# Optimization experiments

Hardware: AMD Instinct MI355X
Metric: run time of the kernel (lower is better)

## Reference

```python
import jax, jax.numpy as jnp
import numpy as np

N, E, T, R, L = 100000, 800000, 2, 4, 2
DIN, H, C, DOUT = 16, 256, 128, 4
EPS = 1e-5


def hetero_linear(x, node_type, W, b):
    # y[i] = x[i] @ W[node_type[i]] + b[node_type[i]]; small fixed T loop
    out = jnp.zeros((x.shape[0], W.shape[-1]), x.dtype)
    for t in range(W.shape[0]):
        out = out + jnp.where((node_type == t)[:, None], x @ W[t] + b[t], jnp.zeros((), x.dtype))
    return out


def hetero_bn(x, node_type, gamma, beta):
    # per-node-type batch norm (training-mode statistics, biased variance)
    T_ = gamma.shape[0]
    cnt = jax.ops.segment_sum(jnp.ones((x.shape[0],), x.dtype), node_type, num_segments=T_)
    cnt = jnp.maximum(cnt, 1.0)[:, None]
    mean = jax.ops.segment_sum(x, node_type, num_segments=T_) / cnt
    var = jax.ops.segment_sum(x * x, node_type, num_segments=T_) / cnt - mean * mean
    inv = jax.lax.rsqrt(var + EPS)
    return (x - mean[node_type]) * inv[node_type] * gamma[node_type] + beta[node_type]


def rgcn_conv(x, edge_index, edge_type, W, root, bias):
    # RGCNConv with sum aggregation: out_i = x_i @ root + b + sum_{(j->i), r} x_j @ W_r
    src, dst = edge_index[0], edge_index[1]
    hs = jnp.einsum('nd,rdf->rnf', x, W)          # [R, N, C]
    msg = hs[edge_type, src]                       # [E, C] per-edge relation-transformed source feats
    agg = jax.ops.segment_sum(msg, dst, num_segments=x.shape[0])
    return agg + x @ root + bias


def setup_inputs() -> dict:
    key = jax.random.key(0)
    ks = iter(jax.random.split(key, 40))

    def w(shape, fan_in):
        return jax.random.normal(next(ks), shape, jnp.float32) / np.float32(np.sqrt(fan_in))

    inp = {}
    inp['x'] = jax.random.normal(next(ks), (N, DIN), jnp.float32)
    inp['edge_index'] = jax.random.randint(next(ks), (2, E), 0, N)
    inp['node_type'] = jax.random.randint(next(ks), (N,), 0, T)
    inp['edge_type'] = jax.random.randint(next(ks), (E,), 0, R)
    inp['ri_w0'] = w((T, DIN, H), DIN); inp['ri_b0'] = jnp.zeros((T, H))
    inp['ri_g0'] = jnp.ones((T, H)); inp['ri_be0'] = jnp.zeros((T, H))
    inp['ri_w1'] = w((T, H, C), H); inp['ri_b1'] = jnp.zeros((T, C))
    inp['cn_g'] = jnp.ones((L, T, C)); inp['cn_b'] = jnp.zeros((L, T, C))
    inp['rg_w'] = w((L, R, C, C), C); inp['rg_root'] = w((L, C, C), C); inp['rg_bias'] = jnp.zeros((L, C))
    inp['mn_g'] = jnp.ones((L, T, C)); inp['mn_b'] = jnp.zeros((L, T, C))
    inp['mw0'] = w((L, T, C, H), C); inp['mb0'] = jnp.zeros((L, T, H))
    inp['mg0'] = jnp.ones((L, T, H)); inp['mbe0'] = jnp.zeros((L, T, H))
    inp['mw1'] = w((L, T, H, C), H); inp['mb1'] = jnp.zeros((L, T, C))
    inp['ro_w0'] = w((T, C, H), C); inp['ro_b0'] = jnp.zeros((T, H))
    inp['ro_g0'] = jnp.ones((T, H)); inp['ro_be0'] = jnp.zeros((T, H))
    inp['ro_w1'] = w((T, H, DOUT), H); inp['ro_b1'] = jnp.zeros((T, DOUT))
    return inp


def reference(x, edge_index, node_type, edge_type,
              ri_w0, ri_b0, ri_g0, ri_be0, ri_w1, ri_b1,
              cn_g, cn_b, rg_w, rg_root, rg_bias,
              mn_g, mn_b, mw0, mb0, mg0, mbe0, mw1, mb1,
              ro_w0, ro_b0, ro_g0, ro_be0, ro_w1, ro_b1):
    act = jax.nn.leaky_relu  # negative_slope 0.01, as nn.LeakyReLU default
    # readin MLP (plain_last)
    h = hetero_linear(x, node_type, ri_w0, ri_b0)
    h = act(hetero_bn(h, node_type, ri_g0, ri_be0))
    h = hetero_linear(h, node_type, ri_w1, ri_b1)
    # RES+ blocks: Norm -> Act -> Conv -> +res, Norm -> Act -> MLP -> +res (dropout=0)
    for l in range(rg_w.shape[0]):
        y = act(hetero_bn(h, node_type, cn_g[l], cn_b[l]))
        h = h + rgcn_conv(y, edge_index, edge_type, rg_w[l], rg_root[l], rg_bias[l])
        y = act(hetero_bn(h, node_type, mn_g[l], mn_b[l]))
        y = hetero_linear(y, node_type, mw0[l], mb0[l])
        y = act(hetero_bn(y, node_type, mg0[l], mbe0[l]))
        y = hetero_linear(y, node_type, mw1[l], mb1[l])
        h = h + y
    # readout MLP (plain_last)
    h = hetero_linear(h, node_type, ro_w0, ro_b0)
    h = act(hetero_bn(h, node_type, ro_g0, ro_be0))
    return hetero_linear(h, node_type, ro_w1, ro_b1)
```

## Files before the change

### kernel.cpp

```cpp
#include <hip/hip_runtime.h>

#define TT 2
#define RR 4
#define LL 2
#define DIN 16
#define HH 256
#define CC 128
#define DOUT 4
#define EPS 1e-5f
#define NB 32
#define NBG 16

typedef float v4f __attribute__((ext_vector_type(4)));
typedef short bf16x8 __attribute__((ext_vector_type(8)));

__device__ __forceinline__ ushort f2bf(float x) {
    uint u = __float_as_uint(x);
    return (ushort)((u + 0x7fffu + ((u >> 16) & 1u)) >> 16);
}
__device__ __forceinline__ float bf2f(ushort h) { return __uint_as_float(((uint)h) << 16); }
__device__ __forceinline__ int swc(int c) { return c ^ ((c >> 3) & 7); }
__device__ __forceinline__ uint pack2(float x, float y) {
    return (uint)f2bf(x) | ((uint)f2bf(y) << 16);
}

__global__ __launch_bounds__(1024) void k_scan1(const int* __restrict__ in, int* __restrict__ out,
                                                int* __restrict__ part, int n) {
    __shared__ int sm[1024];
    const int tid = threadIdx.x;
    const int i = blockIdx.x * 1024 + tid;
    const int v = (i < n) ? in[i] : 0;
    sm[tid] = v;
    __syncthreads();
    for (int off = 1; off < 1024; off <<= 1) {
        const int u = (tid >= off) ? sm[tid - off] : 0;
        __syncthreads();
        sm[tid] += u;
        __syncthreads();
    }
    if (i < n) out[i] = sm[tid] - v;
    if (tid == 1023) part[blockIdx.x] = sm[1023];
}

__global__ __launch_bounds__(1024) void k_scan2(int* __restrict__ part, int nb) {
    __shared__ int sm[1024];
    const int tid = threadIdx.x;
    const int v = (tid < nb) ? part[tid] : 0;
    sm[tid] = v;
    __syncthreads();
    for (int off = 1; off < 1024; off <<= 1) {
        const int u = (tid >= off) ? sm[tid - off] : 0;
        __syncthreads();
        sm[tid] += u;
        __syncthreads();
    }
    if (tid < nb) part[tid] = sm[tid] - v;
    if (tid == nb - 1) part[nb] = sm[tid];
}

__global__ __launch_bounds__(1024) void k_scan3(int* __restrict__ arr, const int* __restrict__ part,
                                                int n, int nb, int* __restrict__ typeStart,
                                                int* __restrict__ out2) {
    const int i = blockIdx.x * 1024 + threadIdx.x;
    if (i < n) {
        const int v = arr[i] + part[i >> 10];
        arr[i] = v;
        if (out2) out2[i] = v;
    } else if (i == n) {
        const int total = part[nb];
        arr[n] = total;
        if (typeStart) { typeStart[0] = 0; typeStart[1] = n - total; typeStart[2] = n; }
    }
}

__global__ __launch_bounds__(256) void k_build_perm(const int* __restrict__ nt, const int* __restrict__ pscan,
                                                    const int* __restrict__ typeStart, int* __restrict__ perm,
                                                    int* __restrict__ inv, int n) {
    const int i = blockIdx.x * 256 + threadIdx.x;
    if (i >= n) return;
    const int s1 = pscan[i];
    const int pos = nt[i] ? (typeStart[1] + s1) : (i - s1);
    perm[pos] = i;
    inv[i] = pos;
}

__global__ __launch_bounds__(256) void k_deg2(const int* __restrict__ dstv, const int* __restrict__ et,
                                              const int* __restrict__ inv, int* __restrict__ rowp2, int nE) {
    const int e = blockIdx.x * 256 + threadIdx.x;
    if (e < nE) atomicAdd(&rowp2[inv[dstv[e]] * 4 + et[e]], 1);
}

__global__ __launch_bounds__(256) void k_fill2(const int* __restrict__ srcv, const int* __restrict__ dstv,
                                               const int* __restrict__ et, const int* __restrict__ inv,
                                               int* __restrict__ cur, int* __restrict__ csr, int nE) {
    const int e = blockIdx.x * 256 + threadIdx.x;
    if (e < nE) {
        const int pos = atomicAdd(&cur[inv[dstv[e]] * 4 + et[e]], 1);
        csr[pos] = inv[srcv[e]];
    }
}

__global__ __launch_bounds__(256) void k_packall(const float* __restrict__ ri_w1, const float* __restrict__ mw0,
                                                 const float* __restrict__ mw1, const float* __restrict__ ro_w0,
                                                 ushort* __restrict__ p_ri1, ushort* __restrict__ p_mw0,
                                                 ushort* __restrict__ p_mw1, ushort* __restrict__ p_ro0) {
    for (long long idx = (long long)blockIdx.x * 256 + threadIdx.x; idx < 393216;
         idx += (long long)gridDim.x * 256) {
        const float* src; ushort* dst; int K, N; long long lo;
        if (idx < 65536)       { src = ri_w1; dst = p_ri1; K = 256; N = 128; lo = idx; }
        else if (idx < 196608) { src = mw0;   dst = p_mw0; K = 128; N = 256; lo = idx - 65536; }
        else if (idx < 327680) { src = mw1;   dst = p_mw1; K = 256; N = 128; lo = idx - 196608; }
        else                   { src = ro_w0; dst = p_ro0; K = 128; N = 256; lo = idx - 327680; }
        const int kn = K * N;
        const int mat = (int)(lo / kn);
        const int rem = (int)(lo - (long long)mat * kn);
        const int k = rem / N, col = rem % N;
        dst[((size_t)mat * (K / 8) + (k >> 3)) * N * 8 + (size_t)col * 8 + (k & 7)] = f2bf(src[lo]);
    }
}

__global__ __launch_bounds__(256) void k_pack_conv(const float* __restrict__ rgw_all,
                                                   const float* __restrict__ root_all,
                                                   ushort* __restrict__ dst_all) {
    const int idx = blockIdx.x * 256 + threadIdx.x;
    if (idx >= 640 * 128) return;
    const int l = blockIdx.y;
    const float* rgw = rgw_all + (size_t)l * RR * CC * CC;
    const float* root = root_all + (size_t)l * CC * CC;
    ushort* dst = dst_all + (size_t)l * 640 * 128;
    const int k = idx >> 7, col = idx & 127;
    const float v = (k < 512) ? rgw[(((k >> 7) * CC) + (k & 127)) * CC + col]
                              : root[(size_t)(k - 512) * CC + col];
    dst[((size_t)(k >> 3) * CC + col) * 8 + (k & 7)] = f2bf(v);
}

__global__ __launch_bounds__(512) void k_coef(const float* __restrict__ stat, const int* __restrict__ typeStart,
                                              const float* __restrict__ g, const float* __restrict__ be,
                                              float* __restrict__ scale, float* __restrict__ shift, int F) {
    const int tid = threadIdx.x;
    if (tid >= TT * F) return;
    const int t = tid / F;
    float s = 0.f, q = 0.f;
    for (int b = 0; b < NB; ++b) {
        s += stat[(size_t)b * 1024 + tid];
        q += stat[(size_t)b * 1024 + 512 + tid];
    }
    const float cnt = fmaxf((float)(typeStart[t + 1] - typeStart[t]), 1.f);
    const float mean = s / cnt;
    const float var = q / cnt - mean * mean;
    const float sc = g[tid] * rsqrtf(var + EPS);
    scale[tid] = sc;
    shift[tid] = be[tid] - mean * sc;
}

__global__ __launch_bounds__(256) void k_bnact(const float* __restrict__ h, const float* __restrict__ stat_in,
                                               const float* __restrict__ gg, const float* __restrict__ bb,
                                               const int* __restrict__ typeStart,
                                               ushort* __restrict__ y16, int n) {
    __shared__ float scs[2 * CC];
    __shared__ float sfs[2 * CC];
    const int tid = threadIdx.x;
    for (int idx = tid; idx < 2 * CC; idx += 256) {
        const int t = idx >> 7;
        float s = 0.f, q = 0.f;
        for (int b = 0; b < NB; ++b) {
            s += stat_in[(size_t)b * 1024 + idx];
            q += stat_in[(size_t)b * 1024 + 512 + idx];
        }
        const float cnt = fmaxf((float)(typeStart[t + 1] - typeStart[t]), 1.f);
        const float mean = s / cnt;
        const float var = q / cnt - mean * mean;
        const float sc = gg[idx] * rsqrtf(var + EPS);
        scs[idx] = sc;
        sfs[idx] = bb[idx] - mean * sc;
    }
    __syncthreads();
    const int c0 = typeStart[1];
    const long long total = (long long)n * 32;
    for (long long idx = (long long)blockIdx.x * 256 + threadIdx.x; idx < total;
         idx += (long long)gridDim.x * 256) {
        const int i = (int)(idx >> 5), cq = (int)(idx & 31);
        const int tb = (i >= c0) ? CC : 0;
        const v4f v = *(const v4f*)(h + (size_t)i * CC + cq * 4);
        float o[4];
#pragma unroll
        for (int j = 0; j < 4; ++j) {
            const float vv = fmaf(v[j], scs[tb + cq * 4 + j], sfs[tb + cq * 4 + j]);
            o[j] = fmaxf(vv, 0.01f * vv);
        }
        uint2 p = make_uint2(pack2(o[0], o[1]), pack2(o[2], o[3]));
        *(uint2*)((uint*)y16 + (size_t)i * 64 + cq * 2) = p;
    }
}

__global__ __launch_bounds__(256) void k_agg4(const ushort* __restrict__ y16, const int* __restrict__ rowp2,
                                              const int* __restrict__ csr, ushort* __restrict__ buf,
                                              int q0, int q1) {
    const int wid = threadIdx.x >> 6, lane = threadIdx.x & 63;
    const int i = q0 + blockIdx.x * 4 + wid;
    if (i >= q1) return;
    const uint* y32 = (const uint*)y16;
    float2 a0 = {0.f, 0.f}, a1 = {0.f, 0.f}, a2 = {0.f, 0.f}, a3 = {0.f, 0.f};
    const int e0 = rowp2[4 * i], b1 = rowp2[4 * i + 1], b2 = rowp2[4 * i + 2],
              b3 = rowp2[4 * i + 3], e1 = rowp2[4 * i + 4];
    for (int base = e0; base < e1; base += 64) {
        const int cnt = min(64, e1 - base);
        int pk = (lane < cnt) ? csr[base + lane] : 0;
        for (int j = 0; j < cnt; j += 8) {
            const int m = min(8, cnt - j);
            uint u[8];
#pragma unroll
            for (int k = 0; k < 8; ++k) {
                if (k < m) {
                    const int s = __shfl(pk, j + k);
                    u[k] = y32[(size_t)s * 64 + lane];
                }
            }
#pragma unroll
            for (int k = 0; k < 8; ++k) {
                if (k < m) {
                    const int idx = base + j + k;
                    const float vx = bf2f((ushort)(u[k] & 0xffff));
                    const float vy = bf2f((ushort)(u[k] >> 16));
                    if (idx < b1)      { a0.x += vx; a0.y += vy; }
                    else if (idx < b2) { a1.x += vx; a1.y += vy; }
                    else if (idx < b3) { a2.x += vx; a2.y += vy; }
                    else               { a3.x += vx; a3.y += vy; }
                }
            }
        }
    }
    uint* brow = (uint*)buf + (size_t)(i - q0) * 256;
    brow[0 * 64 + lane] = pack2(a0.x, a0.y);
    brow[1 * 64 + lane] = pack2(a1.x, a1.y);
    brow[2 * 64 + lane] = pack2(a2.x, a2.y);
    brow[3 * 64 + lane] = pack2(a3.x, a3.y);
}

__global__ __launch_bounds__(256) void k_gram(const float* __restrict__ x, const int* __restrict__ perm,
                                              const int* __restrict__ typeStart, float* __restrict__ gram) {
    __shared__ float Xs[256][17];
    const int tid = threadIdx.x;
    const int t = blockIdx.y;
    const int rbeg = typeStart[t], rend = typeStart[t + 1];
    const int r0 = rbeg + blockIdx.x * 1024;
    if (r0 >= rend) return;
    const int i = tid >> 4, j = tid & 15;
    float acc = 0.f, sacc = 0.f;
    for (int rr = 0; rr < 4; ++rr) {
        const int gr = r0 + rr * 256 + tid;
        v4f x0 = 0.f, x1 = 0.f, x2 = 0.f, x3 = 0.f;
        if (gr < rend) {
            const float* xr = x + (size_t)perm[gr] * DIN;
            x0 = *(const v4f*)xr; x1 = *(const v4f*)(xr + 4);
            x2 = *(const v4f*)(xr + 8); x3 = *(const v4f*)(xr + 12);
        }
        __syncthreads();
#pragma unroll
        for (int e = 0; e < 4; ++e) { Xs[tid][e] = x0[e]; Xs[tid][4 + e] = x1[e];
                                      Xs[tid][8 + e] = x2[e]; Xs[tid][12 + e] = x3[e]; }
        __syncthreads();
        for (int r = 0; r < 256; ++r) acc += Xs[r][i] * Xs[r][j];
        if (tid < 16)
            for (int r = 0; r < 256; ++r) sacc += Xs[r][tid];
        __syncthreads();
    }
    float* gb = gram + ((size_t)t * NBG + (blockIdx.x & (NBG - 1))) * 272;
    atomicAdd(&gb[tid], acc);
    if (tid < 16) atomicAdd(&gb[256 + tid], sacc);
}

__global__ __launch_bounds__(512) void k_ri_coef(const float* __restrict__ gram, const int* __restrict__ typeStart,
                                                 const float* __restrict__ ri_w0, const float* __restrict__ ri_b0,
                                                 const float* __restrict__ g, const float* __restrict__ be,
                                                 float* __restrict__ w0eff, float* __restrict__ b0eff) {
    __shared__ float G[2][272];
    const int tid = threadIdx.x;
    for (int idx = tid; idx < 2 * 272; idx += 512) {
        const int tt = idx / 272, k = idx % 272;
        float s = 0.f;
        for (int b = 0; b < NBG; ++b) s += gram[((size_t)tt * NBG + b) * 272 + k];
        G[tt][k] = s;
    }
    __syncthreads();
    const int t = tid >> 8, c = tid & 255;
    float wv[16];
#pragma unroll
    for (int k = 0; k < 16; ++k) wv[k] = ri_w0[((size_t)t * 16 + k) * HH + c];
    const float b = ri_b0[t * HH + c];
    const float cnt = fmaxf((float)(typeStart[t + 1] - typeStart[t]), 1.f);
    float sw = 0.f;
#pragma unroll
    for (int k = 0; k < 16; ++k) sw += G[t][256 + k] * wv[k];
    const float mean = (sw + cnt * b) / cnt;
    float e2 = 0.f;
#pragma unroll
    for (int i = 0; i < 16; ++i) {
        const float wi = wv[i];
#pragma unroll
        for (int j = 0; j < 16; ++j) e2 += wi * wv[j] * G[t][i * 16 + j];
    }
    e2 = (e2 + 2.f * b * sw + cnt * b * b) / cnt;
    const float var = e2 - mean * mean;
    const float sc = g[t * HH + c] * rsqrtf(var + EPS);
    const float sf = be[t * HH + c] - mean * sc;
    b0eff[t * HH + c] = b * sc + sf;
#pragma unroll
    for (int k = 0; k < 16; ++k) w0eff[((size_t)t * 16 + k) * HH + c] = wv[k] * sc;
}

__global__ __launch_bounds__(256) void k_readin(const float* __restrict__ x, const int* __restrict__ perm,
                                                const int* __restrict__ typeStart,
                                                const float* __restrict__ w0eff, const float* __restrict__ b0eff,
                                                const ushort* __restrict__ Wp, const float* __restrict__ b1,
                                                float* __restrict__ h, ushort* __restrict__ h16,
                                                float* __restrict__ stat) {
    __shared__ float Xs[128][17];
    __shared__ float W0s[16][256];
    __shared__ float b0s[256];
    __shared__ ushort As[128][40];
    __shared__ ushort Ws[4][128][8];

    const int tid = threadIdx.x;
    const int lane = tid & 63;
    const int wid = tid >> 6;
    const int woffm = (wid >> 1) * 64, woffn = (wid & 1) * 64;
    const int t = blockIdx.y;
    const int rbeg = typeStart[t], rend = typeStart[t + 1];
    const int r0 = rbeg + blockIdx.x * 128;
    if (r0 >= rend) return;

    for (int idx = tid; idx < 16 * 256; idx += 256) W0s[idx >> 8][idx & 255] = w0eff[(size_t)t * 4096 + idx];
    if (tid < 256) b0s[tid] = b0eff[t * 256 + tid];

    const int srow = tid >> 1, half = tid & 1;
    const int sgr = r0 + srow;
    const bool svalid = sgr < rend;
    {
        v4f x0 = 0.f, x1 = 0.f;
        if (svalid) {
            const float* xr = x + (size_t)perm[sgr] * DIN + half * 8;
            x0 = *(const v4f*)xr; x1 = *(const v4f*)(xr + 4);
        }
#pragma unroll
        for (int e = 0; e < 4; ++e) { Xs[srow][half * 8 + e] = x0[e]; Xs[srow][half * 8 + 4 + e] = x1[e]; }
    }
    __syncthreads();
    float xr[16];
#pragma unroll
    for (int k = 0; k < 16; ++k) xr[k] = Xs[srow][k];

    v4f acc[4][4];
#pragma unroll
    for (int mt = 0; mt < 4; ++mt)
#pragma unroll
        for (int nt = 0; nt < 4; ++nt) acc[mt][nt] = (v4f){0.f, 0.f, 0.f, 0.f};

    const size_t wmat = (size_t)t * 256 * 128;
    const int wcp = tid & 63;

    for (int kt = 0; kt < 8; ++kt) {
        const int k0 = kt * 32;
        ushort hA[16];
#pragma unroll
        for (int c2 = 0; c2 < 16; ++c2) {
            const int col = k0 + half * 16 + c2;
            float d = b0s[col];
#pragma unroll
            for (int k = 0; k < 16; ++k) d = fmaf(xr[k], W0s[k][col], d);
            d = fmaxf(d, 0.01f * d);
            hA[c2] = f2bf(d);
        }
        const ushort* wsrc = Wp + wmat + ((size_t)(k0 / 8 + wid) * 128) * 8 + (size_t)wcp * 16;
        const uint4 w0 = *(const uint4*)wsrc;
        const uint4 w1 = *(const uint4*)(wsrc + 8);
        __syncthreads();
        *(uint4*)&As[srow][half * 16] = *(uint4*)&hA[0];
        *(uint4*)&As[srow][half * 16 + 8] = *(uint4*)&hA[8];
        *(uint4*)&Ws[wid][swc(wcp * 2)][0] = w0;
        *(uint4*)&Ws[wid][swc(wcp * 2 + 1)][0] = w1;
        __syncthreads();
        const int afr = lane & 15;
        const int akg = (lane >> 4) * 8;
        bf16x8 aF[4], wf[4];
#pragma unroll
        for (int mt = 0; mt < 4; ++mt) aF[mt] = *(const bf16x8*)&As[woffm + mt * 16 + afr][akg];
#pragma unroll
        for (int nt = 0; nt < 4; ++nt) wf[nt] = *(const bf16x8*)&Ws[lane >> 4][swc(woffn + nt * 16 + afr)][0];
#pragma unroll
        for (int mt = 0; mt < 4; ++mt)
#pragma unroll
            for (int nt = 0; nt < 4; ++nt)
                acc[mt][nt] = __builtin_amdgcn_mfma_f32_16x16x32_bf16(aF[mt], wf[nt], acc[mt][nt], 0, 0, 0);
    }

    float bv[4];
#pragma unroll
    for (int nt = 0; nt < 4; ++nt) bv[nt] = b1[t * 128 + woffn + nt * 16 + (lane & 15)];
    float cs[4] = {0.f, 0.f, 0.f, 0.f}, cq[4] = {0.f, 0.f, 0.f, 0.f};
#pragma unroll
    for (int mt = 0; mt < 4; ++mt) {
        const int grow = r0 + woffm + mt * 16 + (lane >> 4) * 4;
#pragma unroll
        for (int nt = 0; nt < 4; ++nt) {
            const int gcol = woffn + nt * 16 + (lane & 15);
#pragma unroll
            for (int rg = 0; rg < 4; ++rg) {
                const int gr = grow + rg;
                if (gr < rend) {
                    const float v = acc[mt][nt][rg] + bv[nt];
                    const size_t o = (size_t)gr * 128 + gcol;
                    h[o] = v;
                    h16[o] = f2bf(v);
                    cs[nt] += v; cq[nt] += v * v;
                }
            }
        }
    }
    float* sb = stat + (size_t)(blockIdx.x & (NB - 1)) * 1024;
#pragma unroll
    for (int nt = 0; nt < 4; ++nt) {
        float s = cs[nt], q = cq[nt];
        s += __shfl_xor(s, 16); q += __shfl_xor(q, 16);
        s += __shfl_xor(s, 32); q += __shfl_xor(q, 32);
        if (lane < 16) {
            const int col = t * 128 + woffn + nt * 16 + lane;
            atomicAdd(&sb[col], s);
            atomicAdd(&sb[512 + col], q);
        }
    }
}

template <int K, int OUTW, bool TYPED, bool WHET, bool CROOT, bool BNIN,
          bool BHET, bool STATS, int OUTMODE>
__global__ __launch_bounds__(256) void k_mf(
    const ushort* __restrict__ Xb, const ushort* __restrict__ Xb2,
    const ushort* __restrict__ Wp, const float* __restrict__ Bb,
    const float* __restrict__ stat_in, const float* __restrict__ gg,
    const float* __restrict__ bb, const int* __restrict__ typeStart,
    float* __restrict__ Y, ushort* __restrict__ Y16, float* __restrict__ stat,
    int rbase, int rbeg_u, int rend_u) {
    constexpr int NT = K / 32;
    constexpr int XSTR = CROOT ? 512 : K;

    __shared__ ushort As[2][64][40];
    __shared__ ushort Ws[2][4][128][8];
    __shared__ float csh[BNIN ? K : 1];
    __shared__ float cfh[BNIN ? K : 1];

    const int tid = threadIdx.x;
    const int lane = tid & 63;
    const int wid = tid >> 6;
    const int kgrp = lane >> 4, fr = lane & 15;
    const int woffm = (wid >> 1) * 32;
    const int woffn = (wid & 1) * 64;

    int t = 0, rbeg = rbeg_u, rend = rend_u;
    if constexpr (TYPED) { t = blockIdx.y; rbeg = typeStart[t]; rend = typeStart[t + 1]; }
    const int r0 = rbeg + blockIdx.x * 64;
    if (r0 >= rend) return;
    const int zoff = (OUTW == 256) ? blockIdx.z * 128 : 0;

    if constexpr (BNIN) {
        const float cnt = fmaxf((float)(typeStart[t + 1] - typeStart[t]), 1.f);
        for (int k = tid; k < K; k += 256) {
            float s = 0.f, q = 0.f;
            for (int b = 0; b < NB; ++b) {
                s += stat_in[(size_t)b * 1024 + t * K + k];
                q += stat_in[(size_t)b * 1024 + 512 + t * K + k];
            }
            const float mean = s / cnt;
            const float var = q / cnt - mean * mean;
            const float sc = gg[t * K + k] * rsqrtf(var + EPS);
            csh[k] = sc;
            cfh[k] = bb[t * K + k] - mean * sc;
        }
        __syncthreads();
    }

    const int srow = tid >> 2, skq = tid & 3;
    const int sgr = r0 + srow;
    const bool sv = sgr < rend;
    const int wcp = tid & 63;
    const size_t wmat = (size_t)(WHET ? t : 0) * K * OUTW;

    auto LOADA = [&](int kt) -> uint4 {
        const int k0 = kt * 32;
        uint4 a = make_uint4(0, 0, 0, 0);
        if (sv) {
            const ushort* p;
            if constexpr (CROOT) {
                p = (k0 >= 512) ? (Xb2 + (size_t)sgr * 128 + (k0 - 512) + skq * 8)
                                : (Xb + (size_t)(sgr - rbase) * XSTR + k0 + skq * 8);
            } else {
                p = Xb + (size_t)(sgr - rbase) * XSTR + k0 + skq * 8;
            }
            a = *(const uint4*)p;
        }
        if constexpr (BNIN) {
            uint ua[4] = {a.x, a.y, a.z, a.w};
#pragma unroll
            for (int e = 0; e < 4; ++e) {
                const int k = kt * 32 + skq * 8 + 2 * e;
                float f0 = fmaf(bf2f((ushort)(ua[e] & 0xffff)), csh[k], cfh[k]);
                float f1 = fmaf(bf2f((ushort)(ua[e] >> 16)), csh[k + 1], cfh[k + 1]);
                f0 = fmaxf(f0, 0.01f * f0);
                f1 = fmaxf(f1, 0.01f * f1);
                ua[e] = pack2(f0, f1);
            }
            a = make_uint4(ua[0], ua[1], ua[2], ua[3]);
        }
        return a;
    };
    auto LOADW = [&](int kt, uint4& w0, uint4& w1) {
        const ushort* wsrc = Wp + wmat + ((size_t)(kt * 4 + wid) * OUTW + zoff) * 8 + (size_t)wcp * 16;
        w0 = *(const uint4*)wsrc;
        w1 = *(const uint4*)(wsrc + 8);
    };
    auto STORE = [&](int b, const uint4& a, const uint4& w0, const uint4& w1) {
        *(uint4*)&As[b][srow][skq * 8] = a;
        *(uint4*)&Ws[b][wid][swc(wcp * 2)][0] = w0;
        *(uint4*)&Ws[b][wid][swc(wcp * 2 + 1)][0] = w1;
    };

    v4f acc[2][4];
#pragma unroll
    for (int mt = 0; mt < 2; ++mt)
#pragma unroll
        for (int nt = 0; nt < 4; ++nt) acc[mt][nt] = (v4f){0.f, 0.f, 0.f, 0.f};

    auto MSTEP = [&](int b) {
        const bf16x8 aF0 = *(const bf16x8*)&As[b][woffm + fr][kgrp * 8];
        const bf16x8 aF1 = *(const bf16x8*)&As[b][woffm + 16 + fr][kgrp * 8];
        bf16x8 wf[4];
#pragma unroll
        for (int nt = 0; nt < 4; ++nt)
            wf[nt] = *(const bf16x8*)&Ws[b][kgrp][swc(woffn + nt * 16 + fr)][0];
#pragma unroll
        for (int nt = 0; nt < 4; ++nt) {
            acc[0][nt] = __builtin_amdgcn_mfma_f32_16x16x32_bf16(aF0, wf[nt], acc[0][nt], 0, 0, 0);
            acc[1][nt] = __builtin_amdgcn_mfma_f32_16x16x32_bf16(aF1, wf[nt], acc[1][nt], 0, 0, 0);
        }
    };

    uint4 aA = make_uint4(0, 0, 0, 0), wA0 = aA, wA1 = aA;
    uint4 aB = aA, wB0 = aA, wB1 = aA;
    {
        uint4 a0 = LOADA(0), w0, w1;
        LOADW(0, w0, w1);
        STORE(0, a0, w0, w1);
    }
    if (NT > 1) { aA = LOADA(1); LOADW(1, wA0, wA1); }
    if (NT > 2) { aB = LOADA(2); LOADW(2, wB0, wB1); }
    __syncthreads();

#pragma unroll
    for (int kt = 0; kt < NT; kt += 2) {
        MSTEP(0);
        {
            STORE(1, aA, wA0, wA1);
            if (kt + 3 < NT) { aA = LOADA(kt + 3); LOADW(kt + 3, wA0, wA1); }
            __syncthreads();
        }
        MSTEP(1);
        if (kt + 2 < NT) {
            STORE(0, aB, wB0, wB1);
            if (kt + 4 < NT) { aB = LOADA(kt + 4); LOADW(kt + 4, wB0, wB1); }
            __syncthreads();
        }
    }

    const float* BbT = Bb + (BHET ? (size_t)t * OUTW : 0);
    float bv[4];
#pragma unroll
    for (int nt = 0; nt < 4; ++nt) bv[nt] = BbT[zoff + woffn + nt * 16 + fr];
    const int c0 = (STATS && !TYPED) ? typeStart[1] : 0;
    float cs0[4] = {0.f, 0.f, 0.f, 0.f}, cq0[4] = {0.f, 0.f, 0.f, 0.f};
    float cs1[4] = {0.f, 0.f, 0.f, 0.f}, cq1[4] = {0.f, 0.f, 0.f, 0.f};
#pragma unroll
    for (int mt = 0; mt < 2; ++mt) {
        const int grow = r0 + woffm + mt * 16 + kgrp * 4;
#pragma unroll
        for (int nt = 0; nt < 4; ++nt) {
            const int gcol = zoff + woffn + nt * 16 + fr;
#pragma unroll
            for (int rg = 0; rg < 4; ++rg) {
                const int gr = grow + rg;
                if (gr < rend) {
                    float v = acc[mt][nt][rg] + bv[nt];
                    const size_t o = (size_t)gr * OUTW + gcol;
                    if constexpr (OUTMODE == 0) Y[o] = v;
                    if constexpr (OUTMODE == 1) Y16[o] = f2bf(v);
                    if constexpr (OUTMODE == 2) {
                        const float hv = Y[o] + v;
                        Y[o] = hv;
                        Y16[o] = f2bf(hv);
                        v = hv;
                    }
                    if constexpr (STATS) {
                        if (TYPED || gr < c0) { cs0[nt] += v; cq0[nt] += v * v; }
                        else                  { cs1[nt] += v; cq1[nt] += v * v; }
                    }
                }
            }
        }
    }
    if constexpr (STATS) {
        float* sb = stat + (size_t)(blockIdx.x & (NB - 1)) * 1024;
#pragma unroll
        for (int nt = 0; nt < 4; ++nt) {
            float s = cs0[nt], q = cq0[nt];
            s += __shfl_xor(s, 16); q += __shfl_xor(q, 16);
            s += __shfl_xor(s, 32); q += __shfl_xor(q, 32);
            if (lane < 16) {
                const int col = t * OUTW + zoff + woffn + nt * 16 + lane;
                atomicAdd(&sb[col], s);
                atomicAdd(&sb[512 + col], q);
            }
            if constexpr (!TYPED) {
                float s1 = cs1[nt], q1 = cq1[nt];
                s1 += __shfl_xor(s1, 16); q1 += __shfl_xor(q1, 16);
                s1 += __shfl_xor(s1, 32); q1 += __shfl_xor(q1, 32);
                if (lane < 16) {
                    const int col = OUTW + zoff + woffn + nt * 16 + lane;
                    atomicAdd(&sb[col], s1);
                    atomicAdd(&sb[512 + col], q1);
                }
            }
        }
    }
}

__global__ __launch_bounds__(256) void k_ro1(const ushort* __restrict__ A256b, const int* __restrict__ perm,
                                             const int* __restrict__ typeStart, const float* __restrict__ ro_w1,
                                             const float* __restrict__ ro_b1, const float* __restrict__ scale,
                                             const float* __restrict__ shift, float* __restrict__ out, int n) {
    __shared__ float W1s[2][256][4];
    __shared__ float scs[512];
    __shared__ float sfs[512];
    const int tid = threadIdx.x;
    for (int idx = tid; idx < 2048; idx += 256) {
        const int t = idx >> 10, rem = idx & 1023;
        W1s[t][rem >> 2][rem & 3] = ro_w1[idx];
    }
    for (int idx = tid; idx < 512; idx += 256) { scs[idx] = scale[idx]; sfs[idx] = shift[idx]; }
    __syncthreads();
    const int trow = tid >> 2, sub = tid & 3;
    const int gr = blockIdx.x * 64 + trow;
    if (gr >= n) return;
    const int c0 = typeStart[1];
    const int t = (gr >= c0) ? 1 : 0;
    v4f acc = 0.f;
    const ushort* ar = A256b + (size_t)gr * 256 + sub * 64;
#pragma unroll
    for (int q = 0; q < 8; ++q) {
        const uint4 u = *(const uint4*)(ar + q * 8);
        const uint uw[4] = {u.x, u.y, u.z, u.w};
#pragma unroll
        for (int e = 0; e < 4; ++e) {
#pragma unroll
            for (int hl = 0; hl < 2; ++hl) {
                const int col = sub * 64 + q * 8 + 2 * e + hl;
                const float v = bf2f((ushort)(hl ? (uw[e] >> 16) : (uw[e] & 0xffff)));
                float vv = fmaf(v, scs[t * 256 + col], sfs[t * 256 + col]);
                vv = fmaxf(vv, 0.01f * vv);
                acc += vv * *(const v4f*)&W1s[t][col][0];
            }
        }
    }
#pragma unroll
    for (int e = 0; e < 4; ++e) { acc[e] += __shfl_xor(acc[e], 1); acc[e] += __shfl_xor(acc[e], 2); }
    if (sub == 0) {
        acc += *(const v4f*)(ro_b1 + t * 4);
        *(v4f*)(out + (size_t)perm[gr] * 4) = acc;
    }
}

extern "C" void kernel_launch(void* const* d_in, const int* in_sizes, int n_in,
                              void* d_out, int out_size, void* d_ws, size_t ws_size,
                              hipStream_t stream) {
    const float* x = (const float*)d_in[0];
    const int* ei = (const int*)d_in[1];
    const int* nt = (const int*)d_in[2];
    const int* et = (const int*)d_in[3];
    const float* ri_w0 = (const float*)d_in[4];
    const float* ri_b0 = (const float*)d_in[5];
    const float* ri_g0 = (const float*)d_in[6];
    const float* ri_be0 = (const float*)d_in[7];
    const float* ri_w1 = (const float*)d_in[8];
    const float* ri_b1 = (const float*)d_in[9];
    const float* cn_g = (const float*)d_in[10];
    const float* cn_b = (const float*)d_in[11];
    const float* rg_w = (const float*)d_in[12];
    const float* rg_root = (const float*)d_in[13];
    const float* rg_bias = (const float*)d_in[14];
    const float* mn_g = (const float*)d_in[15];
    const float* mn_b = (const float*)d_in[16];
    const float* mw0 = (const float*)d_in[17];
    const float* mb0 = (const float*)d_in[18];
    const float* mg0 = (const float*)d_in[19];
    const float* mbe0 = (const float*)d_in[20];
    const float* mw1 = (const float*)d_in[21];
    const float* mb1 = (const float*)d_in[22];
    const float* ro_w0 = (const float*)d_in[23];
    const float* ro_b0 = (const float*)d_in[24];
    const float* ro_g0 = (const float*)d_in[25];
    const float* ro_be0 = (const float*)d_in[26];
    const float* ro_w1 = (const float*)d_in[27];
    const float* ro_b1 = (const float*)d_in[28];

    const int n = in_sizes[2];
    const int nE = in_sizes[3];
    const int* srcv = ei;
    const int* dstv = ei + nE;

    char* w = (char*)d_ws;
    size_t off = 0;
    auto alloc = [&](size_t bytes) -> char* {
        char* p = w + off;
        off = (off + bytes + 255) & ~(size_t)255;
        return p;
    };
    float* h = (float*)alloc((size_t)n * CC * sizeof(float));
    ushort* h16 = (ushort*)alloc((size_t)(n + 128) * CC * sizeof(ushort));
    int* csr = (int*)alloc((size_t)nE * sizeof(int));
    int* rowp2 = (int*)alloc(((size_t)4 * n + 1) * sizeof(int));
    int* cur2 = (int*)alloc((size_t)4 * n * sizeof(int));
    int* perm = (int*)alloc((size_t)n * sizeof(int));
    int* inv = (int*)alloc((size_t)n * sizeof(int));
    int* pscan = (int*)alloc((size_t)(n + 1) * sizeof(int));
    int* part = (int*)alloc(2052 * sizeof(int));
    int* typeStart = (int*)alloc(64);
    float* statgram = (float*)alloc(((size_t)9 * NB * 1024 + 2 * NBG * 272) * sizeof(float));
    float* scale = (float*)alloc(512 * sizeof(float));
    float* shift = (float*)alloc(512 * sizeof(float));
    float* w0eff = (float*)alloc((size_t)2 * 16 * 256 * sizeof(float));
    float* b0eff = (float*)alloc(512 * sizeof(float));
    ushort* pw_ri1 = (ushort*)alloc(65536 * 2);
    ushort* pw_mw0 = (ushort*)alloc(131072 * 2);
    ushort* pw_mw1 = (ushort*)alloc(131072 * 2);
    ushort* pw_ro0 = (ushort*)alloc(65536 * 2);
    ushort* pw_conv = (ushort*)alloc(163840 * 2);
    char* region2 = alloc((size_t)(n + 128) * 512);
    if (ws_size < off) return;

    float* statbuf = statgram;
    float* gram = statgram + (size_t)9 * NB * 1024;
    ushort* A256b = (ushort*)region2;
    ushort* y16 = (ushort*)region2;
    float* out = (float*)d_out;

    ushort* buf = (ushort*)(w + off);
    const size_t bufBytes = (ws_size > off) ? (ws_size - off) : 0;
    const long long chkcap = (long long)(bufBytes / 1024) - 128;
    if (chkcap < 1024) return;
    int nchunk, CHK;
    if (chkcap >= n) { nchunk = 1; CHK = n; }
    else { nchunk = (int)((n + chkcap - 1) / chkcap); CHK = (n + nchunk - 1) / nchunk; }

    auto SS = [&](int slot) { return statbuf + (size_t)slot * NB * 1024; };

    const int gE = (nE + 255) / 256;
    const int gN = (n + 255) / 256;
    const int nb = (n + 1023) / 1024;
    const int m4 = 4 * n;
    const int nb2 = (m4 + 1023) / 1024;
    const int gmx = (n + 127) / 128;
    const int gm64 = (n + 63) / 64;

    k_packall<<<1536, 256, 0, stream>>>(ri_w1, mw0, mw1, ro_w0, pw_ri1, pw_mw0, pw_mw1, pw_ro0);
    k_pack_conv<<<dim3(320, 2), 256, 0, stream>>>(rg_w, rg_root, pw_conv);

    hipMemsetAsync(statgram, 0, ((size_t)9 * NB * 1024 + 2 * NBG * 272) * sizeof(float), stream);
    k_scan1<<<nb, 1024, 0, stream>>>(nt, pscan, part, n);
    k_scan2<<<1, 1024, 0, stream>>>(part, nb);
    k_scan3<<<(n + 1024) / 1024, 1024, 0, stream>>>(pscan, part, n, nb, typeStart, nullptr);
    k_build_perm<<<gN, 256, 0, stream>>>(nt, pscan, typeStart, perm, inv, n);
    hipMemsetAsync(rowp2, 0, ((size_t)m4 + 1) * sizeof(int), stream);
    k_deg2<<<gE, 256, 0, stream>>>(dstv, et, inv, rowp2, nE);
    k_scan1<<<nb2, 1024, 0, stream>>>(rowp2, rowp2, part, m4);
    k_scan2<<<1, 1024, 0, stream>>>(part, nb2);
    k_scan3<<<(m4 + 1024) / 1024, 1024, 0, stream>>>(rowp2, part, m4, nb2, nullptr, cur2);
    k_fill2<<<gE, 256, 0, stream>>>(srcv, dstv, et, inv, cur2, csr, nE);

    k_gram<<<dim3((n + 1023) / 1024, 2), 256, 0, stream>>>(x, perm, typeStart, gram);
    k_ri_coef<<<1, 512, 0, stream>>>(gram, typeStart, ri_w0, ri_b0, ri_g0, ri_be0, w0eff, b0eff);
    k_readin<<<dim3(gmx, 2), 256, 0, stream>>>(x, perm, typeStart, w0eff, b0eff, pw_ri1, ri_b1,
                                               h, h16, SS(1));

    for (int l = 0; l < LL; ++l) {
        const int s_cn = l ? 4 : 1, s_mn = l ? 5 : 2, s_mg = l ? 6 : 3, s_nx = l ? 7 : 4;
        k_bnact<<<1280, 256, 0, stream>>>(h, SS(s_cn), cn_g + (size_t)l * TT * CC,
                                          cn_b + (size_t)l * TT * CC, typeStart, y16, n);
        const ushort* wconv = pw_conv + (size_t)l * 640 * 128;
        for (int q0 = 0; q0 < n; q0 += CHK) {
            const int q1 = min(n, q0 + CHK);
            k_agg4<<<(q1 - q0 + 3) / 4, 256, 0, stream>>>(y16, rowp2, csr, buf, q0, q1);
            k_mf<640, 128, false, false, true, false, false, true, 2>
                <<<(q1 - q0 + 63) / 64, 256, 0, stream>>>(
                    buf, y16, wconv, rg_bias + (size_t)l * CC, nullptr, nullptr, nullptr,
                    typeStart, h, h16, SS(s_mn), q0, q0, q1);
        }

        k_mf<128, 256, true, true, false, true, true, true, 1><<<dim3(gm64, 2, 2), 256, 0, stream>>>(
            h16, nullptr, pw_mw0 + (size_t)l * 2 * 128 * 256, mb0 + (size_t)l * TT * HH,
            SS(s_mn), mn_g + (size_t)l * TT * CC, mn_b + (size_t)l * TT * CC,
            typeStart, nullptr, A256b, SS(s_mg), 0, 0, n);
        if (l == 0)
            k_mf<256, 128, true, true, false, true, true, true, 2><<<dim3(gm64, 2, 1), 256, 0, stream>>>(
                A256b, nullptr, pw_mw1 + (size_t)l * 2 * 256 * 128, mb1 + (size_t)l * TT * CC,
                SS(s_mg), mg0 + (size_t)l * TT * HH, mbe0 + (size_t)l * TT * HH,
                typeStart, h, h16, SS(s_nx), 0, 0, n);
        else
            k_mf<256, 128, true, true, false, true, true, false, 2><<<dim3(gm64, 2, 1), 256, 0, stream>>>(
                A256b, nullptr, pw_mw1 + (size_t)l * 2 * 256 * 128, mb1 + (size_t)l * TT * CC,
                SS(s_mg), mg0 + (size_t)l * TT * HH, mbe0 + (size_t)l * TT * HH,
                typeStart, h, h16, nullptr, 0, 0, n);
    }

    k_mf<128, 256, true, true, false, false, true, true, 1><<<dim3(gm64, 2, 2), 256, 0, stream>>>(
        h16, nullptr, pw_ro0, ro_b0, nullptr, nullptr, nullptr, typeStart, nullptr, A256b, SS(8), 0, 0, n);
    k_coef<<<1, 512, 0, stream>>>(SS(8), typeStart, ro_g0, ro_be0, scale, shift, HH);
    k_ro1<<<(n + 63) / 64, 256, 0, stream>>>(A256b, perm, typeStart, ro_w1, ro_b1, scale, shift, out, n);
}
```

Measured before the change: 707.5 us.

## Fuse edge aggregation into conv GEMM via shared-memory A tile

Merges the per-relation neighbor aggregation kernel and the conv GEMM into a single kernel. Each block aggregates 64 destination rows into a swizzled 64x512 bf16 LDS tile, then runs the MFMA GEMM against it, with the root term read directly from y16. This removes the global round trip through the chunked aggregation buffer and the chunking logic. In exchange, each block uses 64KB of LDS, which lowers occupancy during the latency-bound gather phase, and each wave handles 16 rows serially.

After: 1.040 ms. 1.47x slower.

```diff
diff --git a/kernel.cpp b/kernel.cpp
--- a/kernel.cpp
+++ b/kernel.cpp
@@ -193,48 +193,186 @@
     }
 }
 
-__global__ __launch_bounds__(256) void k_agg4(const ushort* __restrict__ y16, const int* __restrict__ rowp2,
-                                              const int* __restrict__ csr, ushort* __restrict__ buf,
-                                              int q0, int q1) {
-    const int wid = threadIdx.x >> 6, lane = threadIdx.x & 63;
-    const int i = q0 + blockIdx.x * 4 + wid;
-    if (i >= q1) return;
+__global__ __launch_bounds__(256) void k_aggmf(
+    const ushort* __restrict__ y16, const int* __restrict__ rowp2, const int* __restrict__ csr,
+    const ushort* __restrict__ Wp, const float* __restrict__ Bb, const int* __restrict__ typeStart,
+    float* __restrict__ Y, ushort* __restrict__ Y16, float* __restrict__ stat, int n) {
+    __shared__ ushort Ab[64][512];
+    __shared__ ushort Ws[2][4][128][8];
+
+    const int tid = threadIdx.x;
+    const int lane = tid & 63;
+    const int wid = tid >> 6;
+    const int kgrp = lane >> 4, fr = lane & 15;
+    const int r0 = blockIdx.x * 64;
+    if (r0 >= n) return;
+
     const uint* y32 = (const uint*)y16;
-    float2 a0 = {0.f, 0.f}, a1 = {0.f, 0.f}, a2 = {0.f, 0.f}, a3 = {0.f, 0.f};
-    const int e0 = rowp2[4 * i], b1 = rowp2[4 * i + 1], b2 = rowp2[4 * i + 2],
-              b3 = rowp2[4 * i + 3], e1 = rowp2[4 * i + 4];
-    for (int base = e0; base < e1; base += 64) {
-        const int cnt = min(64, e1 - base);
-        int pk = (lane < cnt) ? csr[base + lane] : 0;
-        for (int j = 0; j < cnt; j += 8) {
-            const int m = min(8, cnt - j);
-            uint u[8];
-#pragma unroll
-            for (int k = 0; k < 8; ++k) {
-                if (k < m) {
-                    const int s = __shfl(pk, j + k);
-                    u[k] = y32[(size_t)s * 64 + lane];
+    uint* ab32 = (uint*)&Ab[0][0];
+    const int lq = lane >> 2, lr = lane & 3;
+
+    for (int rr = 0; rr < 16; ++rr) {
+        const int m = wid * 16 + rr;
+        const int i = r0 + m;
+        float2 a0 = {0.f, 0.f}, a1 = {0.f, 0.f}, a2 = {0.f, 0.f}, a3 = {0.f, 0.f};
+        if (i < n) {
+            const int e0 = rowp2[4 * i], b1 = rowp2[4 * i + 1], b2 = rowp2[4 * i + 2],
+                      b3 = rowp2[4 * i + 3], e1 = rowp2[4 * i + 4];
+            for (int base = e0; base < e1; base += 64) {
+                const int cnt = min(64, e1 - base);
+                int pk = (lane < cnt) ? csr[base + lane] : 0;
+                for (int j = 0; j < cnt; j += 8) {
+                    const int mm = min(8, cnt - j);
+                    uint u[8];
+#pragma unroll
+                    for (int k = 0; k < 8; ++k) {
+                        if (k < mm) {
+                            const int s = __shfl(pk, j + k);
+                            u[k] = y32[(size_t)s * 64 + lane];
+                        }
+                    }
+#pragma unroll
+                    for (int k = 0; k < 8; ++k) {
+                        if (k < mm) {
+                            const int idx = base + j + k;
+                            const float vx = bf2f((ushort)(u[k] & 0xffff));
+                            const float vy = bf2f((ushort)(u[k] >> 16));
+                            if (idx < b1)      { a0.x += vx; a0.y += vy; }
+                            else if (idx < b2) { a1.x += vx; a1.y += vy; }
+                            else if (idx < b3) { a2.x += vx; a2.y += vy; }
+                            else               { a3.x += vx; a3.y += vy; }
+                        }
+                    }
                 }
             }
-#pragma unroll
-            for (int k = 0; k < 8; ++k) {
-                if (k < m) {
-                    const int idx = base + j + k;
-                    const float vx = bf2f((ushort)(u[k] & 0xffff));
-                    const float vy = bf2f((ushort)(u[k] >> 16));
-                    if (idx < b1)      { a0.x += vx; a0.y += vy; }
-                    else if (idx < b2) { a1.x += vx; a1.y += vy; }
-                    else if (idx < b3) { a2.x += vx; a2.y += vy; }
-                    else               { a3.x += vx; a3.y += vy; }
+        }
+        const int swz = (m & 7) << 3;
+        ab32[m * 256 + ((lq) ^ swz) * 4 + lr]      = pack2(a0.x, a0.y);
+        ab32[m * 256 + ((16 + lq) ^ swz) * 4 + lr] = pack2(a1.x, a1.y);
+        ab32[m * 256 + ((32 + lq) ^ swz) * 4 + lr] = pack2(a2.x, a2.y);
+        ab32[m * 256 + ((48 + lq) ^ swz) * 4 + lr] = pack2(a3.x, a3.y);
+    }
+
+    const int wcp = tid & 63;
+    const int woffm = (wid >> 1) * 32;
+    const int woffn = (wid & 1) * 64;
+
+    auto LOADW = [&](int kt, uint4& w0, uint4& w1) {
+        const ushort* wsrc = Wp + ((size_t)(kt * 4 + wid) * 128) * 8 + (size_t)wcp * 16;
+        w0 = *(const uint4*)wsrc;
+        w1 = *(const uint4*)(wsrc + 8);
+    };
+    auto STOREW = [&](int b, const uint4& w0, const uint4& w1) {
+        *(uint4*)&Ws[b][wid][swc(wcp * 2)][0] = w0;
+        *(uint4*)&Ws[b][wid][swc(wcp * 2 + 1)][0] = w1;
+    };
+
+    v4f acc[2][4];
+#pragma unroll
+    for (int mt = 0; mt < 2; ++mt)
+#pragma unroll
+        for (int nt = 0; nt < 4; ++nt) acc[mt][nt] = (v4f){0.f, 0.f, 0.f, 0.f};
+
+    uint4 wA0, wA1, wB0, wB1;
+    {
+        uint4 t0, t1;
+        LOADW(0, t0, t1);
+        STOREW(0, t0, t1);
+    }
+    LOADW(1, wA0, wA1);
+    LOADW(2, wB0, wB1);
+    __syncthreads();
+
+    const ushort* abp = (const ushort*)Ab;
+    auto AFRAG = [&](int kt, int mt) -> bf16x8 {
+        const int m = woffm + mt * 16 + fr;
+        if (kt < 16) {
+            const int chunk = (kt * 4 + kgrp) ^ ((m & 7) << 3);
+            return *(const bf16x8*)(abp + (size_t)m * 512 + chunk * 8);
+        } else {
+            const int gr = r0 + m;
+            uint4 a = make_uint4(0, 0, 0, 0);
+            if (gr < n) a = *(const uint4*)(y16 + (size_t)gr * 128 + (kt - 16) * 32 + kgrp * 8);
+            union { uint4 u; bf16x8 b; } cv;
+            cv.u = a;
+            return cv.b;
+        }
+    };
+    auto MSTEP = [&](int b, int kt) {
+        const bf16x8 aF0 = AFRAG(kt, 0);
+        const bf16x8 aF1 = AFRAG(kt, 1);
+        bf16x8 wf[4];
+#pragma unroll
+        for (int nt = 0; nt < 4; ++nt)
+            wf[nt] = *(const bf16x8*)&Ws[b][kgrp][swc(woffn + nt * 16 + fr)][0];
+#pragma unroll
+        for (int nt = 0; nt < 4; ++nt) {
+            acc[0][nt] = __builtin_amdgcn_mfma_f32_16x16x32_bf16(aF0, wf[nt], acc[0][nt], 0, 0, 0);
+            acc[1][nt] = __builtin_amdgcn_mfma_f32_16x16x32_bf16(aF1, wf[nt], acc[1][nt], 0, 0, 0);
+        }
+    };
+
+    for (int kt = 0; kt < 20; kt += 2) {
+        MSTEP(0, kt);
+        STOREW(1, wA0, wA1);
+        if (kt + 3 < 20) LOADW(kt + 3, wA0, wA1);
+        __syncthreads();
+        MSTEP(1, kt + 1);
+        if (kt + 2 < 20) {
+            STOREW(0, wB0, wB1);
+            if (kt + 4 < 20) LOADW(kt + 4, wB0, wB1);
+            __syncthreads();
+        }
+    }
+
+    float bv[4];
+#pragma unroll
+    for (int nt = 0; nt < 4; ++nt) bv[nt] = Bb[woffn + nt * 16 + fr];
+    const int c0 = typeStart[1];
+    float cs0[4] = {0.f, 0.f, 0.f, 0.f}, cq0[4] = {0.f, 0.f, 0.f, 0.f};
+    float cs1[4] = {0.f, 0.f, 0.f, 0.f}, cq1[4] = {0.f, 0.f, 0.f, 0.f};
+#pragma unroll
+    for (int mt = 0; mt < 2; ++mt) {
+        const int grow = r0 + woffm + mt * 16 + kgrp * 4;
+#pragma unroll
+        for (int nt = 0; nt < 4; ++nt) {
+            const int gcol = woffn + nt * 16 + fr;
+#pragma unroll
+            for (int rg = 0; rg < 4; ++rg) {
+                const int gr = grow + rg;
+                if (gr < n) {
+                    float v = acc[mt][nt][rg] + bv[nt];
+                    const size_t o = (size_t)gr * CC + gcol;
+                    const float hv = Y[o] + v;
+                    Y[o] = hv;
+                    Y16[o] = f2bf(hv);
+                    v = hv;
+                    if (gr < c0) { cs0[nt] += v; cq0[nt] += v * v; }
+                    else         { cs1[nt] += v; cq1[nt] += v * v; }
                 }
             }
         }
     }
-    uint* brow = (uint*)buf + (size_t)(i - q0) * 256;
-    brow[0 * 64 + lane] = pack2(a0.x, a0.y);
-    brow[1 * 64 + lane] = pack2(a1.x, a1.y);
-    brow[2 * 64 + lane] = pack2(a2.x, a2.y);
-    brow[3 * 64 + lane] = pack2(a3.x, a3.y);
+    float* sb = stat + (size_t)(blockIdx.x & (NB - 1)) * 1024;
+#pragma unroll
+    for (int nt = 0; nt < 4; ++nt) {
+        float s = cs0[nt], q = cq0[nt];
+        s += __shfl_xor(s, 16); q += __shfl_xor(q, 16);
+        s += __shfl_xor(s, 32); q += __shfl_xor(q, 32);
+        if (lane < 16) {
+            const int col = woffn + nt * 16 + lane;
+            atomicAdd(&sb[col], s);
+            atomicAdd(&sb[512 + col], q);
+        }
+        float s1 = cs1[nt], q1 = cq1[nt];
+        s1 += __shfl_xor(s1, 16); q1 += __shfl_xor(q1, 16);
+        s1 += __shfl_xor(s1, 32); q1 += __shfl_xor(q1, 32);
+        if (lane < 16) {
+            const int col = CC + woffn + nt * 16 + lane;
+            atomicAdd(&sb[col], s1);
+            atomicAdd(&sb[512 + col], q1);
+        }
+    }
 }
 
 __global__ __launch_bounds__(256) void k_gram(const float* __restrict__ x, const int* __restrict__ perm,
@@ -431,17 +569,14 @@
     }
 }
 
-template <int K, int OUTW, bool TYPED, bool WHET, bool CROOT, bool BNIN,
-          bool BHET, bool STATS, int OUTMODE>
+template <int K, int OUTW, bool TYPED, bool WHET, bool BNIN, bool BHET, bool STATS, int OUTMODE>
 __global__ __launch_bounds__(256) void k_mf(
-    const ushort* __restrict__ Xb, const ushort* __restrict__ Xb2,
-    const ushort* __restrict__ Wp, const float* __restrict__ Bb,
+    const ushort* __restrict__ Xb, const ushort* __restrict__ Wp, const float* __restrict__ Bb,
     const float* __restrict__ stat_in, const float* __restrict__ gg,
     const float* __restrict__ bb, const int* __restrict__ typeStart,
     float* __restrict__ Y, ushort* __restrict__ Y16, float* __restrict__ stat,
-    int rbase, int rbeg_u, int rend_u) {
+    int rbeg_u, int rend_u) {
     constexpr int NT = K / 32;
-    constexpr int XSTR = CROOT ? 512 : K;
 
     __shared__ ushort As[2][64][40];
     __shared__ ushort Ws[2][4][128][8];
@@ -487,16 +622,7 @@
     auto LOADA = [&](int kt) -> uint4 {
         const int k0 = kt * 32;
         uint4 a = make_uint4(0, 0, 0, 0);
-        if (sv) {
-            const ushort* p;
-            if constexpr (CROOT) {
-                p = (k0 >= 512) ? (Xb2 + (size_t)sgr * 128 + (k0 - 512) + skq * 8)
-                                : (Xb + (size_t)(sgr - rbase) * XSTR + k0 + skq * 8);
-            } else {
-                p = Xb + (size_t)(sgr - rbase) * XSTR + k0 + skq * 8;
-            }
-            a = *(const uint4*)p;
-        }
+        if (sv) a = *(const uint4*)(Xb + (size_t)sgr * K + k0 + skq * 8);
         if constexpr (BNIN) {
             uint ua[4] = {a.x, a.y, a.z, a.w};
 #pragma unroll
@@ -750,14 +876,6 @@
     ushort* y16 = (ushort*)region2;
     float* out = (float*)d_out;
 
-    ushort* buf = (ushort*)(w + off);
-    const size_t bufBytes = (ws_size > off) ? (ws_size - off) : 0;
-    const long long chkcap = (long long)(bufBytes / 1024) - 128;
-    if (chkcap < 1024) return;
-    int nchunk, CHK;
-    if (chkcap >= n) { nchunk = 1; CHK = n; }
-    else { nchunk = (int)((n + chkcap - 1) / chkcap); CHK = (n + nchunk - 1) / nchunk; }
-
     auto SS = [&](int slot) { return statbuf + (size_t)slot * NB * 1024; };
 
     const int gE = (nE + 255) / 256;
@@ -792,34 +910,27 @@
         const int s_cn = l ? 4 : 1, s_mn = l ? 5 : 2, s_mg = l ? 6 : 3, s_nx = l ? 7 : 4;
         k_bnact<<<1280, 256, 0, stream>>>(h, SS(s_cn), cn_g + (size_t)l * TT * CC,
                                           cn_b + (size_t)l * TT * CC, typeStart, y16, n);
-        const ushort* wconv = pw_conv + (size_t)l * 640 * 128;
-        for (int q0 = 0; q0 < n; q0 += CHK) {
-            const int q1 = min(n, q0 + CHK);
-            k_agg4<<<(q1 - q0 + 3) / 4, 256, 0, stream>>>(y16, rowp2, csr, buf, q0, q1);
-            k_mf<640, 128, false, false, true, false, false, true, 2>
-                <<<(q1 - q0 + 63) / 64, 256, 0, stream>>>(
-                    buf, y16, wconv, rg_bias + (size_t)l * CC, nullptr, nullptr, nullptr,
-                    typeStart, h, h16, SS(s_mn), q0, q0, q1);
-        }
-
-        k_mf<128, 256, true, true, false, true, true, true, 1><<<dim3(gm64, 2, 2), 256, 0, stream>>>(
-            h16, nullptr, pw_mw0 + (size_t)l * 2 * 128 * 256, mb0 + (size_t)l * TT * HH,
+        k_aggmf<<<gm64, 256, 0, stream>>>(y16, rowp2, csr, pw_conv + (size_t)l * 640 * 128,
+                                          rg_bias + (size_t)l * CC, typeStart, h, h16, SS(s_mn), n);
+
+        k_mf<128, 256, true, true, true, true, true, 1><<<dim3(gm64, 2, 2), 256, 0, stream>>>(
+            h16, pw_mw0 + (size_t)l * 2 * 128 * 256, mb0 + (size_t)l * TT * HH,
             SS(s_mn), mn_g + (size_t)l * TT * CC, mn_b + (size_t)l * TT * CC,
-            typeStart, nullptr, A256b, SS(s_mg), 0, 0, n);
+            typeStart, nullptr, A256b, SS(s_mg), 0, n);
         if (l == 0)
-            k_mf<256, 128, true, true, false, true, true, true, 2><<<dim3(gm64, 2, 1), 256, 0, stream>>>(
-                A256b, nullptr, pw_mw1 + (size_t)l * 2 * 256 * 128, mb1 + (size_t)l * TT * CC,
+            k_mf<256, 128, true, true, true, true, true, 2><<<dim3(gm64, 2, 1), 256, 0, stream>>>(
+                A256b, pw_mw1 + (size_t)l * 2 * 256 * 128, mb1 + (size_t)l * TT * CC,
                 SS(s_mg), mg0 + (size_t)l * TT * HH, mbe0 + (size_t)l * TT * HH,
-                typeStart, h, h16, SS(s_nx), 0, 0, n);
+                typeStart, h, h16, SS(s_nx), 0, n);
         else
-            k_mf<256, 128, true, true, false, true, true, false, 2><<<dim3(gm64, 2, 1), 256, 0, stream>>>(
-                A256b, nullptr, pw_mw1 + (size_t)l * 2 * 256 * 128, mb1 + (size_t)l * TT * CC,
+            k_mf<256, 128, true, true, true, true, false, 2><<<dim3(gm64, 2, 1), 256, 0, stream>>>(
+                A256b, pw_mw1 + (size_t)l * 2 * 256 * 128, mb1 + (size_t)l * TT * CC,
                 SS(s_mg), mg0 + (size_t)l * TT * HH, mbe0 + (size_t)l * TT * HH,
-                typeStart, h, h16, nullptr, 0, 0, n);
-    }
-
-    k_mf<128, 256, true, true, false, false, true, true, 1><<<dim3(gm64, 2, 2), 256, 0, stream>>>(
-        h16, nullptr, pw_ro0, ro_b0, nullptr, nullptr, nullptr, typeStart, nullptr, A256b, SS(8), 0, 0, n);
+                typeStart, h, h16, nullptr, 0, n);
+    }
+
+    k_mf<128, 256, true, true, false, true, true, 1><<<dim3(gm64, 2, 2), 256, 0, stream>>>(
+        h16, pw_ro0, ro_b0, nullptr, nullptr, nullptr, typeStart, nullptr, A256b, SS(8), 0, n);
     k_coef<<<1, 512, 0, stream>>>(SS(8), typeStart, ro_g0, ro_be0, scale, shift, HH);
     k_ro1<<<(n + 63) / 64, 256, 0, stream>>>(A256b, perm, typeStart, ro_w1, ro_b1, scale, shift, out, n);
 }
```
